# Optimization experiments

Hardware: AMD Instinct MI355X
Metric: run time of the kernel (lower is better)

Reference implementation:

```python
import jax, jax.numpy as jnp
import numpy as np

B, N, T_FULL, T, KS, FEAT = 32, 360, 512, 64, 8, 8
NLAYERS = 3   # DCGRU layers
GLAYERS = 4   # bidirectional GRU layers in GruKRegion


def _gru_layer(x, Wih, Whh, bih, bhh, reverse):
    # x: [M, Tg, in] -> [M, Tg, H]; PyTorch GRU gate order (r, z, n)
    M = x.shape[0]
    Hh = Whh.shape[1]
    xp = jnp.einsum('mti,gi->mtg', x, Wih) + bih  # precompute input projections
    if reverse:
        xp = xp[:, ::-1]

    def step(h, xg):
        gh = jnp.einsum('mh,gh->mg', h, Whh) + bhh
        xr, xz, xn = jnp.split(xg, 3, -1)
        hr, hz, hn = jnp.split(gh, 3, -1)
        r = jax.nn.sigmoid(xr + hr)
        z = jax.nn.sigmoid(xz + hz)
        n = jnp.tanh(xn + r * hn)
        hnew = (1.0 - z) * n + z * h
        return hnew, hnew

    _, hs = jax.lax.scan(step, jnp.zeros((M, Hh), x.dtype), jnp.swapaxes(xp, 0, 1))
    hs = jnp.swapaxes(hs, 0, 1)
    if reverse:
        hs = hs[:, ::-1]
    return hs


def _dcgru_cell(x, h, adj, gw, gb, cw, cb):
    # x, h: [B, N] (rnn_units = 1); adj: [B, N, N]; max_diffusion_step = 2
    def gconv(inp, st, W, bias):
        x0 = jnp.stack([inp, st], axis=-1)                     # [B,N,2]
        x1 = jnp.einsum('bnm,bmc->bnc', adj, x0)
        x2 = 2.0 * jnp.einsum('bnm,bmc->bnc', adj, x1) - x0    # Chebyshev recurrence
        # torch layout: [B,N,C,num_matrices] flattened channel-major
        xc = jnp.stack([x0, x1, x2], axis=-1).reshape(x0.shape[0], N, 6)
        return jnp.einsum('bnf,fo->bno', xc, W) + bias

    gates = jax.nn.sigmoid(gconv(x, h, gw, gb))                # [B,N,2]
    r, u = gates[..., 0], gates[..., 1]
    c = jnp.tanh(gconv(x, r * h, cw, cb)[..., 0])
    return u * h + (1.0 - u) * c


def _forward(full_seq, reconstruct_seq, node_feas, temperature,
             g0wih, g0whh, g0bih, g0bhh, gwih, gwhh, gbih, gbhh,
             l1w, l1b, l2w, l2b,
             enc_gw, enc_gb, enc_cw, enc_cb,
             dec_gw, dec_gb, dec_cw, dec_cb, proj_w, proj_b):
    b, n, tfull = full_seq.shape
    # ---- GruKRegion feature extractor ----
    x = full_seq.reshape(b * n, tfull // KS, KS)
    out = jnp.concatenate(
        [_gru_layer(x, g0wih[0], g0whh[0], g0bih[0], g0bhh[0], False),
         _gru_layer(x, g0wih[1], g0whh[1], g0bih[1], g0bhh[1], True)], axis=-1)
    for l in range(GLAYERS - 1):
        out = jnp.concatenate(
            [_gru_layer(out, gwih[l, 0], gwhh[l, 0], gbih[l, 0], gbhh[l, 0], False),
             _gru_layer(out, gwih[l, 1], gwhh[l, 1], gbih[l, 1], gbhh[l, 1], True)], axis=-1)
    feat = out[:, -1, :].reshape(b, n, 2 * KS)
    feat = jax.nn.leaky_relu(jnp.einsum('bnf,of->bno', feat, l1w) + l1b, 0.2)
    feat = jnp.einsum('bnf,of->bno', feat, l2w) + l2b          # [B,N,FEAT]
    # ---- Embed2GraphByProduct ----
    logits = jnp.einsum('bjk,bpk->bjp', feat, feat)            # [B,N,N]
    # ---- hard gumbel softmax ----
    U = jax.random.uniform(jax.random.key(42), logits.shape, logits.dtype)
    g = -jnp.log(-jnp.log(U + 1e-10) + 1e-10)
    y_soft = jax.nn.softmax((logits + g) / temperature, axis=-1)
    y_hard = jax.nn.one_hot(jnp.argmax(y_soft, -1), n, dtype=y_soft.dtype)
    adj = y_soft + jax.lax.stop_gradient(y_hard - y_soft)
    adj = jnp.where(jnp.eye(n, dtype=bool), 0.0, adj)          # zero diagonal
    # (original computes a random-walk matrix then discards it; skipped)
    # ---- encoder: scan over time, 3 stacked DCGRU layers ----
    seq = jnp.transpose(reconstruct_seq, (2, 0, 1))            # [T,B,N]

    def enc_step(hid, xt):
        o = xt
        new = []
        for l in range(NLAYERS):
            hnew = _dcgru_cell(o, hid[l], adj, enc_gw[l], enc_gb[l], enc_cw[l], enc_cb[l])
            new.append(hnew)
            o = hnew
        return jnp.stack(new), None

    hid, _ = jax.lax.scan(enc_step, jnp.zeros((NLAYERS, b, n), seq.dtype), seq)

    def dec_step(carry, _):
        hidc, inp = carry
        o = inp
        new = []
        for l in range(NLAYERS):
            hnew = _dcgru_cell(o, hidc[l], adj, dec_gw[l], dec_gb[l], dec_cw[l], dec_cb[l])
            new.append(hnew)
            o = hnew
        proj = o * proj_w[0, 0] + proj_b[0]                    # Linear(1,1)
        return (jnp.stack(new), proj), proj

    _, outs = jax.lax.scan(dec_step, (hid, jnp.zeros((b, n), seq.dtype)), None, length=T)
    return jnp.transpose(outs, (1, 2, 0))                      # [B,N,T]


def setup_inputs():
    key = jax.random.key(0)
    ks = jax.random.split(key, 24)
    s = 0.2
    p = lambda k, sh: jax.random.normal(k, sh, jnp.float32) * s
    return dict(
        full_seq=jax.random.normal(ks[0], (B, N, T_FULL), jnp.float32),
        reconstruct_seq=jax.random.normal(ks[1], (B, N, T), jnp.float32),
        node_feas=jax.random.normal(ks[2], (B, N, KS), jnp.float32),
        temperature=jnp.ones((), jnp.float32),
        g0wih=p(ks[3], (2, 3 * KS, KS)), g0whh=p(ks[4], (2, 3 * KS, KS)),
        g0bih=p(ks[5], (2, 3 * KS)), g0bhh=p(ks[6], (2, 3 * KS)),
        gwih=p(ks[7], (GLAYERS - 1, 2, 3 * KS, 2 * KS)),
        gwhh=p(ks[8], (GLAYERS - 1, 2, 3 * KS, KS)),
        gbih=p(ks[9], (GLAYERS - 1, 2, 3 * KS)), gbhh=p(ks[10], (GLAYERS - 1, 2, 3 * KS)),
        l1w=p(ks[11], (KS, 2 * KS)), l1b=p(ks[12], (KS,)),
        l2w=p(ks[13], (FEAT, KS)), l2b=p(ks[14], (FEAT,)),
        enc_gw=p(ks[15], (NLAYERS, 6, 2)), enc_gb=jnp.ones((NLAYERS, 2), jnp.float32),
        enc_cw=p(ks[16], (NLAYERS, 6, 1)), enc_cb=jnp.zeros((NLAYERS, 1), jnp.float32),
        dec_gw=p(ks[17], (NLAYERS, 6, 2)), dec_gb=jnp.ones((NLAYERS, 2), jnp.float32),
        dec_cw=p(ks[18], (NLAYERS, 6, 1)), dec_cb=jnp.zeros((NLAYERS, 1), jnp.float32),
        proj_w=p(ks[19], (1, 1)), proj_b=jnp.zeros((1,), jnp.float32),
    )


def reference(full_seq, reconstruct_seq, node_feas, temperature,
              g0wih, g0whh, g0bih, g0bhh, gwih, gwhh, gbih, gbhh,
              l1w, l1b, l2w, l2b,
              enc_gw, enc_gb, enc_cw, enc_cb,
              dec_gw, dec_gb, dec_cw, dec_cb, proj_w, proj_b):
    return _forward(full_seq, reconstruct_seq, node_feas, temperature,
                    g0wih, g0whh, g0bih, g0bhh, gwih, gwhh, gbih, gbhh,
                    l1w, l1b, l2w, l2b,
                    enc_gw, enc_gb, enc_cw, enc_cb,
                    dec_gw, dec_gb, dec_cw, dec_cb, proj_w, proj_b)
```

## Files before the change

### kernel.cpp

```cpp
#include <hip/hip_runtime.h>
#include <math.h>

#define M_SEQ 11520
#define NNODE 360
#define NB    32
#define TT    64

__device__ __forceinline__ float fsigd(float x)  { return 1.0f / (1.0f + __expf(-x)); }
__device__ __forceinline__ float ftanhd(float x) { return 1.0f - 2.0f / (__expf(2.0f * x) + 1.0f); }

__device__ __forceinline__ unsigned rotl32(unsigned x, int n) { return (x << n) | (x >> (32 - n)); }

__device__ __forceinline__ void tf2x32(unsigned& x0, unsigned& x1)
{
    const unsigned k0 = 0u, k1 = 42u, k2 = 0u ^ 42u ^ 0x1BD11BDAu;
    x0 += k0; x1 += k1;
#define R4(a,b,c,d) \
    x0 += x1; x1 = rotl32(x1,a); x1 ^= x0; \
    x0 += x1; x1 = rotl32(x1,b); x1 ^= x0; \
    x0 += x1; x1 = rotl32(x1,c); x1 ^= x0; \
    x0 += x1; x1 = rotl32(x1,d); x1 ^= x0;
    R4(13,15,26,6)   x0 += k1; x1 += k2 + 1u;
    R4(17,29,16,24)  x0 += k2; x1 += k0 + 2u;
    R4(13,15,26,6)   x0 += k0; x1 += k1 + 3u;
    R4(17,29,16,24)  x0 += k1; x1 += k2 + 4u;
    R4(13,15,26,6)   x0 += k2; x1 += k0 + 5u;
#undef R4
}

__device__ __forceinline__ float jax_uniform(unsigned idx)
{
    unsigned x0 = 0u, x1 = idx;
    tf2x32(x0, x1);
    unsigned bits = x0 ^ x1;
    return __uint_as_float((bits >> 9) | 0x3f800000u) - 1.0f;
}

template<int K>
__device__ __forceinline__ void swz_fma(float h, const float* w0, const float* w1,
                                        const float* w2, float& g0, float& g1, float& g2)
{
    float hk = __int_as_float(
        __builtin_amdgcn_ds_swizzle(__float_as_int(h), (K << 5) | 0x18));
    g0 += hk * w0[K];
    g1 += hk * w1[K];
    g2 += hk * w2[K];
    if constexpr (K < 7)
        swz_fma<K + 1>(h, w0, w1, w2, g0, g1, g2);
}

template<int I>
__device__ __forceinline__ void ldx(float* __restrict__ xv, const float* __restrict__ p)
{
    const float4* p4 = reinterpret_cast<const float4*>(p);
#pragma unroll
    for (int q = 0; q < I / 4; ++q) {
        float4 f = p4[q];
        xv[4*q] = f.x; xv[4*q+1] = f.y; xv[4*q+2] = f.z; xv[4*q+3] = f.w;
    }
}

template<int I>
__device__ __forceinline__ void xgates(const float* __restrict__ xv,
    const float* wx0, const float* wx1, const float* wx2,
    float bx0, float bx1, float bx2, float& xr, float& xz, float& xn)
{
    xr = bx0; xz = bx1; xn = bx2;
#pragma unroll
    for (int k = 0; k < I; ++k) {
        xr += xv[k] * wx0[k];
        xz += xv[k] * wx1[k];
        xn += xv[k] * wx2[k];
    }
}

__device__ __forceinline__ float hstep(float h, float xr, float xz, float xn,
    const float* w0, const float* w1, const float* w2,
    float bh0, float bh1, float bh2)
{
    float gh0 = bh0, gh1 = bh1, gh2 = bh2;
    swz_fma<0>(h, w0, w1, w2, gh0, gh1, gh2);
    float r  = fsigd(xr + gh0);
    float z  = fsigd(xz + gh1);
    float nn = ftanhd(xn + r * gh2);
    return (1.f - z) * nn + z * h;
}

template<int I>
__global__ __launch_bounds__(256) void gru_fused(
    const float* __restrict__ x,
    const float* __restrict__ wih,
    const float* __restrict__ whh,
    const float* __restrict__ bih,
    const float* __restrict__ bhh,
    float* __restrict__ out)
{
    const int tid = blockIdx.x * 256 + threadIdx.x;
    const int j   = tid & 7;
    const int md  = tid >> 3;
    if (md >= M_SEQ * 2) return;
    const int m = md >> 1, dir = md & 1;

    float wx0[I], wx1[I], wx2[I];
    const float* WI = wih + dir * 24 * I;
#pragma unroll
    for (int k = 0; k < I; ++k) {
        wx0[k] = WI[j * I + k];
        wx1[k] = WI[(8 + j) * I + k];
        wx2[k] = WI[(16 + j) * I + k];
    }
    float w0[8], w1[8], w2[8];
    const float* WH = whh + dir * 192;
#pragma unroll
    for (int k = 0; k < 8; ++k) {
        w0[k] = WH[j * 8 + k];
        w1[k] = WH[(8 + j) * 8 + k];
        w2[k] = WH[(16 + j) * 8 + k];
    }
    const float bx0 = bih[dir*24 + j], bx1 = bih[dir*24 + 8 + j], bx2 = bih[dir*24 + 16 + j];
    const float bh0 = bhh[dir*24 + j], bh1 = bhh[dir*24 + 8 + j], bh2 = bhh[dir*24 + 16 + j];

    const float* xm = x + (size_t)m * TT * I;
    float* om = out + (size_t)m * TT * 16 + dir * 8 + j;

    const int tstep = dir ? -1 : 1;
    const int tbase = dir ? TT - 1 : 0;

    float h = 0.f;
    float xva[I], xvb[I];
    ldx<I>(xva, xm + (tbase) * I);
    ldx<I>(xvb, xm + (tbase + tstep) * I);
    float cr, cz, cn;
    xgates<I>(xva, wx0, wx1, wx2, bx0, bx1, bx2, cr, cz, cn);

    for (int tt = 0; tt < TT; tt += 2) {
        const int t0 = tbase + tstep * tt;
        const int t1 = t0 + tstep;
        if (tt + 2 < TT) ldx<I>(xva, xm + (t0 + 2 * tstep) * I);
        float nr, nz, nn;
        xgates<I>(xvb, wx0, wx1, wx2, bx0, bx1, bx2, nr, nz, nn);
        h = hstep(h, cr, cz, cn, w0, w1, w2, bh0, bh1, bh2);
        om[t0 * 16] = h;
        if (tt + 3 < TT) ldx<I>(xvb, xm + (t0 + 3 * tstep) * I);
        h = hstep(h, nr, nz, nn, w0, w1, w2, bh0, bh1, bh2);
        om[t1 * 16] = h;
        xgates<I>(xva, wx0, wx1, wx2, bx0, bx1, bx2, cr, cz, cn);
    }
}

__global__ void feat_kernel(const float* __restrict__ gout,
                            const float* __restrict__ l1w, const float* __restrict__ l1b,
                            const float* __restrict__ l2w, const float* __restrict__ l2b,
                            float* __restrict__ feat)
{
    int m = blockIdx.x * blockDim.x + threadIdx.x;
    if (m >= M_SEQ) return;
    const float* xp = gout + (size_t)m * TT * 16 + (TT - 1) * 16;
    float xv[16];
#pragma unroll
    for (int i = 0; i < 16; ++i) xv[i] = xp[i];
    float h1[8];
#pragma unroll
    for (int o = 0; o < 8; ++o) {
        float a = 0.f;
#pragma unroll
        for (int f = 0; f < 16; ++f) a += xv[f] * l1w[o * 16 + f];
        a += l1b[o];
        h1[o] = (a >= 0.f) ? a : 0.2f * a;
    }
#pragma unroll
    for (int o = 0; o < 8; ++o) {
        float a = 0.f;
#pragma unroll
        for (int f = 0; f < 8; ++f) a += h1[f] * l2w[o * 8 + f];
        feat[(size_t)m * 8 + o] = a + l2b[o];
    }
}

__global__ void adj_kernel(const float* __restrict__ feat,
                           const float* __restrict__ tptr,
                           int* __restrict__ colp, float* __restrict__ vp)
{
    const int gw   = (blockIdx.x * blockDim.x + threadIdx.x) >> 6;
    const int lane = threadIdx.x & 63;
    if (gw >= NB * NNODE) return;
    const int b = gw / NNODE;
    const int n = gw - b * NNODE;
    const float T = tptr[0];
    const float* fb = feat + (size_t)b * NNODE * 8;
    float fn[8];
#pragma unroll
    for (int k = 0; k < 8; ++k) fn[k] = fb[(size_t)n * 8 + k];

    float sv[6];
    float mval = -3.0e38f; int midx = 1 << 30;
#pragma unroll
    for (int s = 0; s < 6; ++s) {
        int p = s * 64 + lane;
        float xs = -3.0e38f;
        if (p < NNODE) {
            const float* fp = fb + (size_t)p * 8;
            float d = 0.f;
#pragma unroll
            for (int k = 0; k < 8; ++k) d += fn[k] * fp[k];
            unsigned idx = (unsigned)gw * 360u + (unsigned)p;
            float u   = jax_uniform(idx);
            float gum = -logf(-logf(u + 1e-10f) + 1e-10f);
            xs = (d + gum) / T;
            if (xs > mval) { mval = xs; midx = p; }
        }
        sv[s] = xs;
    }
    for (int off = 32; off > 0; off >>= 1) {
        float ov = __shfl_xor(mval, off);
        int   oi = __shfl_xor(midx, off);
        if (ov > mval || (ov == mval && oi < midx)) { mval = ov; midx = oi; }
    }
    float ssum = 0.f;
#pragma unroll
    for (int s = 0; s < 6; ++s) {
        int p = s * 64 + lane;
        if (p < NNODE) ssum += expf(sv[s] - mval);
    }
    for (int off = 32; off > 0; off >>= 1) ssum += __shfl_xor(ssum, off);
    if (lane == 0) {
        float ys = 1.0f / ssum;
        float v  = ys + (1.0f - ys);
        if (midx == n) v = 0.0f;
        colp[gw] = midx;
        vp[gw]   = v;
    }
}

__device__ __forceinline__ float run3(
    float* __restrict__ s_o, float (* __restrict__ s_h)[NNODE],
    float* __restrict__ s_rh,
    const float* __restrict__ Wg, const float* __restrict__ Bg,
    const float* __restrict__ Wc, const float* __restrict__ Cb,
    bool act, int n, int c1, int c2, float v, float vv,
    float* __restrict__ hreg, float o)
{
#pragma unroll
    for (int l = 0; l < 3; ++l) {
        __syncthreads();
        float oc1 = 0.f, oc2 = 0.f, hc1 = 0.f, hc2 = 0.f;
        if (act) {
            oc1 = s_o[c1]; oc2 = s_o[c2];
            hc1 = s_h[l][c1]; hc2 = s_h[l][c2];
        }
        const float hn = hreg[l];
        const float* W = Wg + l * 12;
        const float bgr = Bg[2 * l], bgu = Bg[2 * l + 1];
        float f1 = v * oc1, f2 = vv * oc2 - o;
        float f4 = v * hc1, f5 = vv * hc2 - hn;
        float r = fsigd(o*W[0] + f1*W[2] + f2*W[4] + hn*W[6] + f4*W[8] + f5*W[10] + bgr);
        float u = fsigd(o*W[1] + f1*W[3] + f2*W[5] + hn*W[7] + f4*W[9] + f5*W[11] + bgu);
        float rhn = r * hn;
        if (act) s_rh[n] = rhn;
        __syncthreads();
        float rhc1 = 0.f, rhc2 = 0.f;
        if (act) { rhc1 = s_rh[c1]; rhc2 = s_rh[c2]; }
        const float* C = Wc + l * 6;
        float cnd = ftanhd(o*C[0] + f1*C[1] + f2*C[2]
                           + rhn*C[3] + (v*rhc1)*C[4] + (vv*rhc2 - rhn)*C[5] + Cb[l]);
        float hnew = u * hn + (1.f - u) * cnd;
        hreg[l] = hnew;
        if (act) { s_h[l][n] = hnew; if (l < 2) s_o[n] = hnew; }
        o = hnew;
    }
    return o;
}

__global__ __launch_bounds__(384) void decode_kernel(
    const float* __restrict__ rec,
    const int*   __restrict__ colp, const float* __restrict__ vp,
    const float* __restrict__ egw, const float* __restrict__ egb,
    const float* __restrict__ ecw, const float* __restrict__ ecb,
    const float* __restrict__ dgw, const float* __restrict__ dgb,
    const float* __restrict__ dcw, const float* __restrict__ dcb,
    const float* __restrict__ pw,  const float* __restrict__ pb,
    float* __restrict__ outp)
{
    __shared__ float s_o[NNODE];
    __shared__ float s_h[3][NNODE];
    __shared__ float s_rh[NNODE];
    __shared__ float s_v[NNODE];
    __shared__ int   s_c[NNODE];
    __shared__ float s_egw[36], s_egb[6], s_ecw[18], s_ecb[3];
    __shared__ float s_dgw[36], s_dgb[6], s_dcw[18], s_dcb[3];

    const int b = blockIdx.x;
    const int n = threadIdx.x;
    if (n < 36) { s_egw[n] = egw[n]; s_dgw[n] = dgw[n]; }
    if (n < 6)  { s_egb[n] = egb[n]; s_dgb[n] = dgb[n]; }
    if (n < 18) { s_ecw[n] = ecw[n]; s_dcw[n] = dcw[n]; }
    if (n < 3)  { s_ecb[n] = ecb[n]; s_dcb[n] = dcb[n]; }
    const bool act = n < NNODE;
    if (act) {
        s_c[n] = colp[b * NNODE + n];
        s_v[n] = vp[b * NNODE + n];
        s_h[0][n] = 0.f; s_h[1][n] = 0.f; s_h[2][n] = 0.f;
    }
    __syncthreads();
    int c1 = 0, c2 = 0; float v = 0.f, vv = 0.f;
    if (act) {
        c1 = s_c[n];
        c2 = s_c[c1];
        v  = s_v[n];
        vv = 2.f * v * s_v[c1];
    }
    const float projw = pw[0], projb = pb[0];
    float hreg[3] = {0.f, 0.f, 0.f};

    float inp = act ? rec[((size_t)b * NNODE + n) * TT + 0] : 0.f;
    for (int t = 0; t < TT; ++t) {
        float nx = (act && t + 1 < TT) ? rec[((size_t)b * NNODE + n) * TT + t + 1] : 0.f;
        if (act) s_o[n] = inp;
        run3(s_o, s_h, s_rh, s_egw, s_egb, s_ecw, s_ecb, act, n, c1, c2, v, vv, hreg, inp);
        inp = nx;
    }
    float dinp = 0.f;
    for (int t = 0; t < TT; ++t) {
        if (act) s_o[n] = dinp;
        float h3 = run3(s_o, s_h, s_rh, s_dgw, s_dgb, s_dcw, s_dcb,
                        act, n, c1, c2, v, vv, hreg, dinp);
        float proj = h3 * projw + projb;
        if (act) outp[((size_t)b * NNODE + n) * TT + t] = proj;
        dinp = proj;
    }
}

extern "C" void kernel_launch(void* const* d_in, const int* in_sizes, int n_in,
                              void* d_out, int out_size, void* d_ws, size_t ws_size,
                              hipStream_t stream)
{
    (void)in_sizes; (void)n_in; (void)out_size; (void)ws_size;
    const float* full_seq = (const float*)d_in[0];
    const float* rec_seq  = (const float*)d_in[1];
    const float* temp     = (const float*)d_in[3];
    const float* g0wih    = (const float*)d_in[4];
    const float* g0whh    = (const float*)d_in[5];
    const float* g0bih    = (const float*)d_in[6];
    const float* g0bhh    = (const float*)d_in[7];
    const float* gwih     = (const float*)d_in[8];
    const float* gwhh     = (const float*)d_in[9];
    const float* gbih     = (const float*)d_in[10];
    const float* gbhh     = (const float*)d_in[11];
    const float* l1w      = (const float*)d_in[12];
    const float* l1b      = (const float*)d_in[13];
    const float* l2w      = (const float*)d_in[14];
    const float* l2b      = (const float*)d_in[15];
    const float* enc_gw   = (const float*)d_in[16];
    const float* enc_gb   = (const float*)d_in[17];
    const float* enc_cw   = (const float*)d_in[18];
    const float* enc_cb   = (const float*)d_in[19];
    const float* dec_gw   = (const float*)d_in[20];
    const float* dec_gb   = (const float*)d_in[21];
    const float* dec_cw   = (const float*)d_in[22];
    const float* dec_cb   = (const float*)d_in[23];
    const float* proj_w   = (const float*)d_in[24];
    const float* proj_b   = (const float*)d_in[25];
    float* outp = (float*)d_out;

    float* ws   = (float*)d_ws;
    float* feat = ws;
    float* vbuf = feat + (size_t)M_SEQ * 8;
    int*   cbuf = (int*)(vbuf + M_SEQ);
    float* bufA = (float*)(cbuf + M_SEQ);
    float* bufB = bufA + (size_t)M_SEQ * TT * 16;

    const int ggru = (M_SEQ * 2 * 8) / 256;
    gru_fused<8><<<ggru, 256, 0, stream>>>(full_seq, g0wih, g0whh, g0bih, g0bhh, bufA);
    gru_fused<16><<<ggru, 256, 0, stream>>>(bufA, gwih + 0 * 768, gwhh + 0 * 384,
                                            gbih + 0 * 48, gbhh + 0 * 48, bufB);
    gru_fused<16><<<ggru, 256, 0, stream>>>(bufB, gwih + 1 * 768, gwhh + 1 * 384,
                                            gbih + 1 * 48, gbhh + 1 * 48, bufA);
    gru_fused<16><<<ggru, 256, 0, stream>>>(bufA, gwih + 2 * 768, gwhh + 2 * 384,
                                            gbih + 2 * 48, gbhh + 2 * 48, bufB);
    feat_kernel<<<M_SEQ / 256, 256, 0, stream>>>(bufB, l1w, l1b, l2w, l2b, feat);
    adj_kernel<<<(NB * NNODE) / 4, 256, 0, stream>>>(feat, temp, cbuf, vbuf);
    decode_kernel<<<NB, 384, 0, stream>>>(rec_seq, cbuf, vbuf,
                                          enc_gw, enc_gb, enc_cw, enc_cb,
                                          dec_gw, dec_gb, dec_cw, dec_cb,
                                          proj_w, proj_b, outp);
}
```

Baseline: 563.5 us.

## Fuse all four bidirectional GRU layers and feature MLP into one kernel using LDS

Replaces four per-layer GRU launches plus the feature kernel with a single kernel where each 128-thread block processes 8 sequences through all layers. Intermediate layer outputs stay in shared memory (two 32KB ping-pong buffers) instead of round-tripping large global buffers. This removes the global memory traffic and launch overhead, but the 64KB of LDS per block and the smaller block size may limit occupancy.

```diff
diff --git a/kernel.cpp b/kernel.cpp
--- a/kernel.cpp
+++ b/kernel.cpp
@@ -5,6 +5,7 @@
 #define NNODE 360
 #define NB    32
 #define TT    64
+#define MPB   8
 
 __device__ __forceinline__ float fsigd(float x)  { return 1.0f / (1.0f + __expf(-x)); }
 __device__ __forceinline__ float ftanhd(float x) { return 1.0f - 2.0f / (__expf(2.0f * x) + 1.0f); }
@@ -86,94 +87,142 @@
     return (1.f - z) * nn + z * h;
 }
 
-template<int I>
-__global__ __launch_bounds__(256) void gru_fused(
-    const float* __restrict__ x,
-    const float* __restrict__ wih,
-    const float* __restrict__ whh,
-    const float* __restrict__ bih,
-    const float* __restrict__ bhh,
-    float* __restrict__ out)
-{
-    const int tid = blockIdx.x * 256 + threadIdx.x;
-    const int j   = tid & 7;
-    const int md  = tid >> 3;
-    if (md >= M_SEQ * 2) return;
-    const int m = md >> 1, dir = md & 1;
-
-    float wx0[I], wx1[I], wx2[I];
-    const float* WI = wih + dir * 24 * I;
-#pragma unroll
-    for (int k = 0; k < I; ++k) {
-        wx0[k] = WI[j * I + k];
-        wx1[k] = WI[(8 + j) * I + k];
-        wx2[k] = WI[(16 + j) * I + k];
-    }
-    float w0[8], w1[8], w2[8];
-    const float* WH = whh + dir * 192;
-#pragma unroll
-    for (int k = 0; k < 8; ++k) {
-        w0[k] = WH[j * 8 + k];
-        w1[k] = WH[(8 + j) * 8 + k];
-        w2[k] = WH[(16 + j) * 8 + k];
-    }
-    const float bx0 = bih[dir*24 + j], bx1 = bih[dir*24 + 8 + j], bx2 = bih[dir*24 + 16 + j];
-    const float bh0 = bhh[dir*24 + j], bh1 = bhh[dir*24 + 8 + j], bh2 = bhh[dir*24 + 16 + j];
-
-    const float* xm = x + (size_t)m * TT * I;
-    float* om = out + (size_t)m * TT * 16 + dir * 8 + j;
-
-    const int tstep = dir ? -1 : 1;
-    const int tbase = dir ? TT - 1 : 0;
-
+template<int I, class LDF, class STF>
+__device__ __forceinline__ void scan_seq(
+    LDF ld, STF st,
+    const float* wx0, const float* wx1, const float* wx2,
+    float bx0, float bx1, float bx2,
+    const float* w0, const float* w1, const float* w2,
+    float bh0, float bh1, float bh2,
+    int tbase, int tstep)
+{
     float h = 0.f;
     float xva[I], xvb[I];
-    ldx<I>(xva, xm + (tbase) * I);
-    ldx<I>(xvb, xm + (tbase + tstep) * I);
+    ld(xva, tbase);
+    ld(xvb, tbase + tstep);
     float cr, cz, cn;
     xgates<I>(xva, wx0, wx1, wx2, bx0, bx1, bx2, cr, cz, cn);
-
     for (int tt = 0; tt < TT; tt += 2) {
         const int t0 = tbase + tstep * tt;
         const int t1 = t0 + tstep;
-        if (tt + 2 < TT) ldx<I>(xva, xm + (t0 + 2 * tstep) * I);
+        if (tt + 2 < TT) ld(xva, t0 + 2 * tstep);
         float nr, nz, nn;
         xgates<I>(xvb, wx0, wx1, wx2, bx0, bx1, bx2, nr, nz, nn);
         h = hstep(h, cr, cz, cn, w0, w1, w2, bh0, bh1, bh2);
-        om[t0 * 16] = h;
-        if (tt + 3 < TT) ldx<I>(xvb, xm + (t0 + 3 * tstep) * I);
+        st(t0, h);
+        if (tt + 3 < TT) ld(xvb, t0 + 3 * tstep);
         h = hstep(h, nr, nz, nn, w0, w1, w2, bh0, bh1, bh2);
-        om[t1 * 16] = h;
+        st(t1, h);
         xgates<I>(xva, wx0, wx1, wx2, bx0, bx1, bx2, cr, cz, cn);
     }
 }
 
-__global__ void feat_kernel(const float* __restrict__ gout,
-                            const float* __restrict__ l1w, const float* __restrict__ l1b,
-                            const float* __restrict__ l2w, const float* __restrict__ l2b,
-                            float* __restrict__ feat)
-{
-    int m = blockIdx.x * blockDim.x + threadIdx.x;
-    if (m >= M_SEQ) return;
-    const float* xp = gout + (size_t)m * TT * 16 + (TT - 1) * 16;
-    float xv[16];
-#pragma unroll
-    for (int i = 0; i < 16; ++i) xv[i] = xp[i];
-    float h1[8];
-#pragma unroll
-    for (int o = 0; o < 8; ++o) {
-        float a = 0.f;
-#pragma unroll
-        for (int f = 0; f < 16; ++f) a += xv[f] * l1w[o * 16 + f];
-        a += l1b[o];
-        h1[o] = (a >= 0.f) ? a : 0.2f * a;
-    }
-#pragma unroll
-    for (int o = 0; o < 8; ++o) {
-        float a = 0.f;
-#pragma unroll
-        for (int f = 0; f < 8; ++f) a += h1[f] * l2w[o * 8 + f];
-        feat[(size_t)m * 8 + o] = a + l2b[o];
+__global__ __launch_bounds__(128) void gru_all(
+    const float* __restrict__ x,
+    const float* __restrict__ g0wih, const float* __restrict__ g0whh,
+    const float* __restrict__ g0bih, const float* __restrict__ g0bhh,
+    const float* __restrict__ gwih,  const float* __restrict__ gwhh,
+    const float* __restrict__ gbih,  const float* __restrict__ gbhh,
+    const float* __restrict__ l1w, const float* __restrict__ l1b,
+    const float* __restrict__ l2w, const float* __restrict__ l2b,
+    float* __restrict__ feat)
+{
+    __shared__ float bufA[TT * MPB * 16];
+    __shared__ float bufB[TT * MPB * 16];
+
+    const int tid  = threadIdx.x;
+    const int j    = tid & 7;
+    const int md   = tid >> 3;
+    const int mloc = md >> 1;
+    const int dir  = md & 1;
+    const int m    = blockIdx.x * MPB + mloc;
+
+    const int tstep = dir ? -1 : 1;
+    const int tbase = dir ? TT - 1 : 0;
+
+    float wx0[16], wx1[16], wx2[16];
+    float w0[8], w1[8], w2[8];
+
+    {
+        const float* WI = g0wih + dir * 24 * 8;
+#pragma unroll
+        for (int k = 0; k < 8; ++k) {
+            wx0[k] = WI[j * 8 + k];
+            wx1[k] = WI[(8 + j) * 8 + k];
+            wx2[k] = WI[(16 + j) * 8 + k];
+        }
+        const float* WH = g0whh + dir * 192;
+#pragma unroll
+        for (int k = 0; k < 8; ++k) {
+            w0[k] = WH[j * 8 + k];
+            w1[k] = WH[(8 + j) * 8 + k];
+            w2[k] = WH[(16 + j) * 8 + k];
+        }
+        const float bx0 = g0bih[dir*24 + j], bx1 = g0bih[dir*24 + 8 + j], bx2 = g0bih[dir*24 + 16 + j];
+        const float bh0 = g0bhh[dir*24 + j], bh1 = g0bhh[dir*24 + 8 + j], bh2 = g0bhh[dir*24 + 16 + j];
+        const float* xm = x + (size_t)m * TT * 8;
+        float* ob = bufA + mloc * 16 + dir * 8 + j;
+        scan_seq<8>(
+            [&](float* xv, int t) { ldx<8>(xv, xm + t * 8); },
+            [&](int t, float h)   { ob[t * (MPB * 16)] = h; },
+            wx0, wx1, wx2, bx0, bx1, bx2, w0, w1, w2, bh0, bh1, bh2, tbase, tstep);
+    }
+    __syncthreads();
+
+    const float* inb = bufA;
+    float*      outb = bufB;
+#pragma unroll 1
+    for (int l = 0; l < 3; ++l) {
+        const float* WI = gwih + l * 768 + dir * 384;
+#pragma unroll
+        for (int k = 0; k < 16; ++k) {
+            wx0[k] = WI[j * 16 + k];
+            wx1[k] = WI[(8 + j) * 16 + k];
+            wx2[k] = WI[(16 + j) * 16 + k];
+        }
+        const float* WH = gwhh + l * 384 + dir * 192;
+#pragma unroll
+        for (int k = 0; k < 8; ++k) {
+            w0[k] = WH[j * 8 + k];
+            w1[k] = WH[(8 + j) * 8 + k];
+            w2[k] = WH[(16 + j) * 8 + k];
+        }
+        const float* BI = gbih + l * 48 + dir * 24;
+        const float* BH = gbhh + l * 48 + dir * 24;
+        const float bx0 = BI[j], bx1 = BI[8 + j], bx2 = BI[16 + j];
+        const float bh0 = BH[j], bh1 = BH[8 + j], bh2 = BH[16 + j];
+        const float* ib = inb + mloc * 16;
+        float*       ob = outb + mloc * 16 + dir * 8 + j;
+        scan_seq<16>(
+            [&](float* xv, int t) { ldx<16>(xv, ib + t * (MPB * 16)); },
+            [&](int t, float h)   { ob[t * (MPB * 16)] = h; },
+            wx0, wx1, wx2, bx0, bx1, bx2, w0, w1, w2, bh0, bh1, bh2, tbase, tstep);
+        __syncthreads();
+        const float* tp = inb; inb = outb; outb = (float*)tp;
+    }
+
+    if (tid < MPB) {
+        const float* xp = inb + (TT - 1) * (MPB * 16) + tid * 16;
+        float xv[16];
+#pragma unroll
+        for (int i = 0; i < 16; ++i) xv[i] = xp[i];
+        float h1[8];
+#pragma unroll
+        for (int o = 0; o < 8; ++o) {
+            float a = 0.f;
+#pragma unroll
+            for (int f = 0; f < 16; ++f) a += xv[f] * l1w[o * 16 + f];
+            a += l1b[o];
+            h1[o] = (a >= 0.f) ? a : 0.2f * a;
+        }
+        const int mg = blockIdx.x * MPB + tid;
+#pragma unroll
+        for (int o = 0; o < 8; ++o) {
+            float a = 0.f;
+#pragma unroll
+            for (int f = 0; f < 8; ++f) a += h1[f] * l2w[o * 8 + f];
+            feat[(size_t)mg * 8 + o] = a + l2b[o];
+        }
     }
 }
 
@@ -366,18 +415,11 @@
     float* feat = ws;
     float* vbuf = feat + (size_t)M_SEQ * 8;
     int*   cbuf = (int*)(vbuf + M_SEQ);
-    float* bufA = (float*)(cbuf + M_SEQ);
-    float* bufB = bufA + (size_t)M_SEQ * TT * 16;
-
-    const int ggru = (M_SEQ * 2 * 8) / 256;
-    gru_fused<8><<<ggru, 256, 0, stream>>>(full_seq, g0wih, g0whh, g0bih, g0bhh, bufA);
-    gru_fused<16><<<ggru, 256, 0, stream>>>(bufA, gwih + 0 * 768, gwhh + 0 * 384,
-                                            gbih + 0 * 48, gbhh + 0 * 48, bufB);
-    gru_fused<16><<<ggru, 256, 0, stream>>>(bufB, gwih + 1 * 768, gwhh + 1 * 384,
-                                            gbih + 1 * 48, gbhh + 1 * 48, bufA);
-    gru_fused<16><<<ggru, 256, 0, stream>>>(bufA, gwih + 2 * 768, gwhh + 2 * 384,
-                                            gbih + 2 * 48, gbhh + 2 * 48, bufB);
-    feat_kernel<<<M_SEQ / 256, 256, 0, stream>>>(bufB, l1w, l1b, l2w, l2b, feat);
+
+    gru_all<<<M_SEQ / MPB, 128, 0, stream>>>(full_seq,
+                                             g0wih, g0whh, g0bih, g0bhh,
+                                             gwih, gwhh, gbih, gbhh,
+                                             l1w, l1b, l2w, l2b, feat);
     adj_kernel<<<(NB * NNODE) / 4, 256, 0, stream>>>(feat, temp, cbuf, vbuf);
     decode_kernel<<<NB, 384, 0, stream>>>(rec_seq, cbuf, vbuf,
                                           enc_gw, enc_gb, enc_cw, enc_cb,
```

New measurement: 644.5 us. +14.4%, slower.
